# Performance work log

Measured on AMD Instinct MI355X. Metric: run time of the kernel, lower is better.

Reference implementation:

```python
import jax, jax.numpy as jnp
import numpy as np


def setup_inputs() -> dict:
    key = jax.random.key(0)
    k1, k2 = jax.random.split(key)
    B, N, M, D = 8, 4096, 4096, 128
    points1 = jax.random.normal(k1, (B, N, D), dtype=jnp.float32)
    points2 = jax.random.normal(k2, (B, M, D), dtype=jnp.float32)
    return {"points1": points1, "points2": points2}


def reference(points1, points2):
    # sum((x[:, :, None] - y[:, None, :])**2, -1), expressed as a GEMM).
    sq1 = jnp.sum(points1 * points1, axis=-1)              # [B, N]
    sq2 = jnp.sum(points2 * points2, axis=-1)              # [B, M]
    cross = jnp.einsum("bnd,bmd->bnm", points1, points2)   # [B, N, M]
    dist_matrix = sq1[:, :, None] + sq2[:, None, :] - 2.0 * cross
    min_dist1 = jnp.min(dist_matrix, axis=2)               # [B, N]
    min_dist2 = jnp.min(dist_matrix, axis=1)               # [B, M]
    return jnp.mean(min_dist1) + jnp.mean(min_dist2)
```

## Files before the change

### kernel.cpp

```cpp
#include <hip/hip_runtime.h>
#include <hip/hip_bf16.h>


#define BATCH 8
#define NPTS 4096
#define DIM 128
#define FBIAS 16384.0f

using bf16x8 = __attribute__((ext_vector_type(8))) short;
using f32x16 = __attribute__((ext_vector_type(16))) float;

__global__ void prep_kernel(const float* __restrict__ p1,
                            const float* __restrict__ p2,
                            __hip_bfloat16* __restrict__ b1,
                            __hip_bfloat16* __restrict__ b2,
                            float* __restrict__ s1,
                            float* __restrict__ s2) {
    const int arr = blockIdx.y;
    const float* src = arr ? p2 : p1;
    __hip_bfloat16* dst = arr ? b2 : b1;
    float* sq = arr ? s2 : s1;
    const float scale = arr ? 1.0f : -2.0f;

    const int wid = threadIdx.x >> 6;
    const int l   = threadIdx.x & 63;
    const int p   = blockIdx.x * 4 + wid;
    const float2 v = *reinterpret_cast<const float2*>(src + (size_t)p * DIM + l * 2);
    float s = v.x * v.x + v.y * v.y;
    __hip_bfloat162 h = __float22bfloat162_rn(make_float2(v.x * scale, v.y * scale));
    *reinterpret_cast<__hip_bfloat162*>(dst + (size_t)p * DIM + l * 2) = h;
    #pragma unroll
    for (int off = 1; off < 64; off <<= 1) s += __shfl_xor(s, off);
    if (l == 0) sq[p] = s;
}

__device__ __forceinline__ void stage16(const __hip_bfloat16* g, void* lds) {
    __builtin_amdgcn_global_load_lds(
        (const __attribute__((address_space(1))) void*)g,
        (__attribute__((address_space(3))) void*)lds, 16, 0, 0);
}

__global__ void __launch_bounds__(256, 4)
chamfer_tile_kernel(const __hip_bfloat16* __restrict__ bf1,
                    const __hip_bfloat16* __restrict__ bf2,
                    const float* __restrict__ sq1,
                    const float* __restrict__ sq2,
                    unsigned int* __restrict__ min1u,
                    unsigned int* __restrict__ min2u) {
    const int lin = blockIdx.x;
    const int b   = lin & 7;
    const int rest = lin >> 3;
    const int nt  = rest & 31;
    const int mh  = rest >> 5;
    const int tid = threadIdx.x;
    const int wid = tid >> 6;
    const int l   = tid & 63;
    const int l31 = l & 31;
    const int lh  = l >> 5;
    const int base = mh * 1024;

    __shared__ __align__(16) unsigned char btile[2][64 * 256];
    __shared__ unsigned int colminu[1024];

    const __hip_bfloat16* bf1b = bf1 + (size_t)b * NPTS * DIM;
    const __hip_bfloat16* bf2b = bf2 + (size_t)b * NPTS * DIM;
    const float* sq1b = sq1 + b * NPTS;
    const float* sq2b = sq2 + b * NPTS;

    const int n0 = nt * 128 + wid * 32;

    bf16x8 afrag[8];
    #pragma unroll
    for (int ks = 0; ks < 8; ++ks)
        afrag[ks] = *reinterpret_cast<const bf16x8*>(
            bf1b + (n0 + l31) * DIM + ks * 16 + lh * 8);

    float sq1v[16];
    #pragma unroll
    for (int reg = 0; reg < 16; ++reg)
        sq1v[reg] = sq1b[n0 + (reg & 3) + 8 * (reg >> 2) + 4 * lh];

    float rmin[16];
    #pragma unroll
    for (int reg = 0; reg < 16; ++reg) rmin[reg] = 3.4e38f;

    const int bofs = l31 * 256 + ((lh * 16) ^ ((l & 1) << 4));
    const int vks  = (l & 14) << 4;

    auto STAGE = [&](int buf, int m0) {
        #pragma unroll
        for (int j = 0; j < 4; ++j) {
            const int c   = j * 256 + wid * 64 + l;
            const int row = c >> 4;
            const int q   = c & 15;
            const __hip_bfloat16* src =
                bf2b + (size_t)(m0 + row) * DIM + (q ^ (row & 15)) * 8;
            stage16(src, &btile[buf][c * 16]);
        }
    };

    auto TAIL = [&](float cp0, float cp1, int mtIdx) {
        float v0 = fminf(cp0, __shfl_xor(cp0, 32));
        float v1 = fminf(cp1, __shfl_xor(cp1, 32));
        if (l < 32) {
            atomicMin(&colminu[mtIdx * 64 + l], __float_as_uint(v0 + FBIAS));
            atomicMin(&colminu[mtIdx * 64 + 32 + l], __float_as_uint(v1 + FBIAS));
        }
    };

    #pragma unroll
    for (int i = 0; i < 4; ++i) colminu[i * 256 + tid] = 0xFFFFFFFFu;
    STAGE(0, base);

    float cp0 = 3.4e38f, cp1 = 3.4e38f;
    int cur = 0;

    for (int mt = 0; mt < 16; ++mt) {
        const int m0 = base + mt * 64;

        asm volatile("s_barrier" ::: "memory");
        if (mt < 15) STAGE(cur ^ 1, m0 + 64);
        if (mt > 0)  TAIL(cp0, cp1, mt - 1);
        if (mt < 15) asm volatile("s_waitcnt vmcnt(4)\n\ts_barrier" ::: "memory");
        else         asm volatile("s_waitcnt vmcnt(0)\n\ts_barrier" ::: "memory");

        f32x16 acc0 = {}, acc1 = {};
        const unsigned char* bt = &btile[cur][0];
        #pragma unroll
        for (int ks = 0; ks < 8; ++ks) {
            const int ko = ((ks * 32) ^ vks);
            bf16x8 b0 = *reinterpret_cast<const bf16x8*>(&bt[bofs + ko]);
            bf16x8 b1 = *reinterpret_cast<const bf16x8*>(&bt[bofs + ko + 8192]);
            acc0 = __builtin_amdgcn_mfma_f32_32x32x16_bf16(afrag[ks], b0, acc0, 0, 0, 0);
            acc1 = __builtin_amdgcn_mfma_f32_32x32x16_bf16(afrag[ks], b1, acc1, 0, 0, 0);
        }

        const float s2v0 = sq2b[m0 + l31];
        const float s2v1 = sq2b[m0 + 32 + l31];
        #pragma unroll
        for (int reg = 0; reg < 16; ++reg)
            rmin[reg] = fminf(rmin[reg],
                              fminf(acc0[reg] + s2v0, acc1[reg] + s2v1));

        float c0 = 3.4e38f, c1 = 3.4e38f;
        #pragma unroll
        for (int reg = 0; reg < 16; reg += 2) {
            c0 = fminf(c0, fminf(acc0[reg] + sq1v[reg],
                                 acc0[reg + 1] + sq1v[reg + 1]));
            c1 = fminf(c1, fminf(acc1[reg] + sq1v[reg],
                                 acc1[reg + 1] + sq1v[reg + 1]));
        }
        cp0 = c0; cp1 = c1;
        cur ^= 1;
    }

    TAIL(cp0, cp1, 15);
    __syncthreads();

    #pragma unroll
    for (int i = 0; i < 4; ++i) {
        const int c = i * 256 + tid;
        atomicMin(&min2u[(size_t)b * NPTS + base + c], colminu[c]);
    }

    #pragma unroll
    for (int reg = 0; reg < 16; ++reg) {
        float v = rmin[reg];
        v = fminf(v, __shfl_xor(v, 1));
        v = fminf(v, __shfl_xor(v, 2));
        v = fminf(v, __shfl_xor(v, 4));
        v = fminf(v, __shfl_xor(v, 8));
        v = fminf(v, __shfl_xor(v, 16));
        rmin[reg] = v;
    }
    if (l31 == 0) {
        #pragma unroll
        for (int reg = 0; reg < 16; ++reg) {
            const int row = n0 + (reg & 3) + 8 * (reg >> 2) + 4 * lh;
            atomicMin(&min1u[(size_t)b * NPTS + row],
                      __float_as_uint(rmin[reg] + FBIAS));
        }
    }
}

__global__ void finalize_kernel(const unsigned int* __restrict__ min1u,
                                const unsigned int* __restrict__ min2u,
                                const float* __restrict__ sq1,
                                const float* __restrict__ sq2,
                                float* __restrict__ out) {
    const int tid = threadIdx.x;
    const int gid = blockIdx.x * 256 + tid;
    float sum;

    if (gid < BATCH * NPTS) {
        sum = (__uint_as_float(min1u[gid]) - FBIAS + sq1[gid])
              * (1.0f / (BATCH * NPTS));
    } else {
        const int idx = gid - BATCH * NPTS;
        sum = (__uint_as_float(min2u[idx]) - FBIAS + sq2[idx])
              * (1.0f / (BATCH * NPTS));
    }

    #pragma unroll
    for (int off = 1; off < 64; off <<= 1) sum += __shfl_xor(sum, off);
    __shared__ float wsum[4];
    if ((tid & 63) == 0) wsum[tid >> 6] = sum;
    __syncthreads();
    if (tid == 0) atomicAdd(out, wsum[0] + wsum[1] + wsum[2] + wsum[3]);
}

extern "C" void kernel_launch(void* const* d_in, const int* in_sizes, int n_in,
                              void* d_out, int out_size, void* d_ws, size_t ws_size,
                              hipStream_t stream) {
    const float* p1 = (const float*)d_in[0];
    const float* p2 = (const float*)d_in[1];
    float* out = (float*)d_out;

    const size_t npts_tot = (size_t)BATCH * NPTS;
    __hip_bfloat16* bf1 = (__hip_bfloat16*)d_ws;
    __hip_bfloat16* bf2 = bf1 + npts_tot * DIM;
    float* sq1 = (float*)(bf2 + npts_tot * DIM);
    float* sq2 = sq1 + npts_tot;
    unsigned int* min1u = (unsigned int*)(sq2 + npts_tot);
    unsigned int* min2u = min1u + npts_tot;

    hipMemsetAsync(d_out, 0, sizeof(float), stream);
    hipMemsetAsync(min1u, 0xFF, npts_tot * 2 * sizeof(unsigned int), stream);

    prep_kernel<<<dim3(npts_tot / 4, 2), 256, 0, stream>>>(p1, p2, bf1, bf2, sq1, sq2);

    chamfer_tile_kernel<<<1024, 256, 0, stream>>>(bf1, bf2, sq1, sq2, min1u, min2u);

    finalize_kernel<<<256, 256, 0, stream>>>(min1u, min2u, sq1, sq2, out);
}
```

Measured before the change: 138.8 us.

## Fold squared norms into GEMM via augmented K dimension, drop memsets

Pads each point row from 128 to 144 bf16 values. The extra slots hold the squared norm as a bf16 hi/lo pair plus ones, so the MFMA computes the full distance directly. This removes the per-element sq1/sq2 adds and loads in the epilogue, folds the memset initialisation into the prep kernel, and simplifies finalize. The cost is 12.5% more MFMA work and traffic, an unswizzled LDS layout with a 288-byte row stride that may raise bank conflicts, and some loss of precision from the bf16 split norms.

```diff
diff --git a/kernel.cpp b/kernel.cpp
--- a/kernel.cpp
+++ b/kernel.cpp
@@ -5,6 +5,8 @@
 #define BATCH 8
 #define NPTS 4096
 #define DIM 128
+#define DIME 144
+#define ROWB 288
 #define FBIAS 16384.0f
 
 using bf16x8 = __attribute__((ext_vector_type(8))) short;
@@ -14,27 +16,49 @@
                             const float* __restrict__ p2,
                             __hip_bfloat16* __restrict__ b1,
                             __hip_bfloat16* __restrict__ b2,
-                            float* __restrict__ s1,
-                            float* __restrict__ s2) {
+                            unsigned int* __restrict__ minAll,
+                            float* __restrict__ out) {
     const int arr = blockIdx.y;
     const float* src = arr ? p2 : p1;
     __hip_bfloat16* dst = arr ? b2 : b1;
-    float* sq = arr ? s2 : s1;
     const float scale = arr ? 1.0f : -2.0f;
 
     const int wid = threadIdx.x >> 6;
     const int l   = threadIdx.x & 63;
     const int p   = blockIdx.x * 4 + wid;
+
     const float2 v = *reinterpret_cast<const float2*>(src + (size_t)p * DIM + l * 2);
     float s = v.x * v.x + v.y * v.y;
     __hip_bfloat162 h = __float22bfloat162_rn(make_float2(v.x * scale, v.y * scale));
-    *reinterpret_cast<__hip_bfloat162*>(dst + (size_t)p * DIM + l * 2) = h;
+    *reinterpret_cast<__hip_bfloat162*>(dst + (size_t)p * DIME + l * 2) = h;
     #pragma unroll
     for (int off = 1; off < 64; off <<= 1) s += __shfl_xor(s, off);
-    if (l == 0) sq[p] = s;
-}
-
-__device__ __forceinline__ void stage16(const __hip_bfloat16* g, void* lds) {
+
+    if (l < 8) {
+        const __hip_bfloat16 shi = __float2bfloat16(s);
+        const __hip_bfloat16 slo = __float2bfloat16(s - __bfloat162float(shi));
+        const __hip_bfloat16 one = __float2bfloat16(1.0f);
+        const __hip_bfloat16 zero = __float2bfloat16(0.0f);
+        __hip_bfloat16 a = zero, bb = zero;
+        if (arr == 0) {
+            if (l == 0) { a = shi; bb = slo; }
+            else if (l == 1) { a = one; bb = one; }
+        } else {
+            if (l == 0) { a = one; bb = one; }
+            else if (l == 1) { a = shi; bb = slo; }
+        }
+        __hip_bfloat162 pair; pair.x = a; pair.y = bb;
+        *reinterpret_cast<__hip_bfloat162*>(dst + (size_t)p * DIME + DIM + l * 2) = pair;
+    }
+
+    if (arr == 0) {
+        if (threadIdx.x < 8)
+            minAll[blockIdx.x * 8 + threadIdx.x] = 0xFFFFFFFFu;
+        if (blockIdx.x == 0 && threadIdx.x == 0) out[0] = 0.0f;
+    }
+}
+
+__device__ __forceinline__ void stage16(const void* g, void* lds) {
     __builtin_amdgcn_global_load_lds(
         (const __attribute__((address_space(1))) void*)g,
         (__attribute__((address_space(3))) void*)lds, 16, 0, 0);
@@ -43,8 +67,6 @@
 __global__ void __launch_bounds__(256, 4)
 chamfer_tile_kernel(const __hip_bfloat16* __restrict__ bf1,
                     const __hip_bfloat16* __restrict__ bf2,
-                    const float* __restrict__ sq1,
-                    const float* __restrict__ sq2,
                     unsigned int* __restrict__ min1u,
                     unsigned int* __restrict__ min2u) {
     const int lin = blockIdx.x;
@@ -59,43 +81,33 @@
     const int lh  = l >> 5;
     const int base = mh * 1024;
 
-    __shared__ __align__(16) unsigned char btile[2][64 * 256];
+    __shared__ __align__(16) unsigned char btile[2][64 * ROWB];
     __shared__ unsigned int colminu[1024];
 
-    const __hip_bfloat16* bf1b = bf1 + (size_t)b * NPTS * DIM;
-    const __hip_bfloat16* bf2b = bf2 + (size_t)b * NPTS * DIM;
-    const float* sq1b = sq1 + b * NPTS;
-    const float* sq2b = sq2 + b * NPTS;
+    const unsigned char* bf1b = (const unsigned char*)(bf1) + (size_t)b * NPTS * ROWB;
+    const unsigned char* bf2b = (const unsigned char*)(bf2) + (size_t)b * NPTS * ROWB;
 
     const int n0 = nt * 128 + wid * 32;
 
-    bf16x8 afrag[8];
-    #pragma unroll
-    for (int ks = 0; ks < 8; ++ks)
+    bf16x8 afrag[9];
+    #pragma unroll
+    for (int ks = 0; ks < 9; ++ks)
         afrag[ks] = *reinterpret_cast<const bf16x8*>(
-            bf1b + (n0 + l31) * DIM + ks * 16 + lh * 8);
-
-    float sq1v[16];
-    #pragma unroll
-    for (int reg = 0; reg < 16; ++reg)
-        sq1v[reg] = sq1b[n0 + (reg & 3) + 8 * (reg >> 2) + 4 * lh];
+            bf1b + (size_t)(n0 + l31) * ROWB + ks * 32 + lh * 16);
 
     float rmin[16];
     #pragma unroll
     for (int reg = 0; reg < 16; ++reg) rmin[reg] = 3.4e38f;
 
-    const int bofs = l31 * 256 + ((lh * 16) ^ ((l & 1) << 4));
-    const int vks  = (l & 14) << 4;
+    const int bofs = l31 * ROWB + lh * 16;
 
     auto STAGE = [&](int buf, int m0) {
-        #pragma unroll
-        for (int j = 0; j < 4; ++j) {
-            const int c   = j * 256 + wid * 64 + l;
-            const int row = c >> 4;
-            const int q   = c & 15;
-            const __hip_bfloat16* src =
-                bf2b + (size_t)(m0 + row) * DIM + (q ^ (row & 15)) * 8;
-            stage16(src, &btile[buf][c * 16]);
+        const unsigned char* tb = bf2b + (size_t)m0 * ROWB;
+        #pragma unroll
+        for (int j = 0; j < 5; ++j) {
+            int c = j * 256 + tid;
+            c = (c >= 1152) ? (c - 1152) : c;
+            stage16(tb + c * 16, &btile[buf][c * 16]);
         }
     };
 
@@ -121,36 +133,34 @@
         asm volatile("s_barrier" ::: "memory");
         if (mt < 15) STAGE(cur ^ 1, m0 + 64);
         if (mt > 0)  TAIL(cp0, cp1, mt - 1);
-        if (mt < 15) asm volatile("s_waitcnt vmcnt(4)\n\ts_barrier" ::: "memory");
+        if (mt < 15) asm volatile("s_waitcnt vmcnt(5)\n\ts_barrier" ::: "memory");
         else         asm volatile("s_waitcnt vmcnt(0)\n\ts_barrier" ::: "memory");
 
         f32x16 acc0 = {}, acc1 = {};
         const unsigned char* bt = &btile[cur][0];
         #pragma unroll
-        for (int ks = 0; ks < 8; ++ks) {
-            const int ko = ((ks * 32) ^ vks);
-            bf16x8 b0 = *reinterpret_cast<const bf16x8*>(&bt[bofs + ko]);
-            bf16x8 b1 = *reinterpret_cast<const bf16x8*>(&bt[bofs + ko + 8192]);
+        for (int ks = 0; ks < 9; ++ks) {
+            bf16x8 b0 = *reinterpret_cast<const bf16x8*>(&bt[bofs + ks * 32]);
+            bf16x8 b1 = *reinterpret_cast<const bf16x8*>(&bt[bofs + ks * 32 + 32 * ROWB]);
             acc0 = __builtin_amdgcn_mfma_f32_32x32x16_bf16(afrag[ks], b0, acc0, 0, 0, 0);
             acc1 = __builtin_amdgcn_mfma_f32_32x32x16_bf16(afrag[ks], b1, acc1, 0, 0, 0);
         }
 
-        const float s2v0 = sq2b[m0 + l31];
-        const float s2v1 = sq2b[m0 + 32 + l31];
         #pragma unroll
         for (int reg = 0; reg < 16; ++reg)
-            rmin[reg] = fminf(rmin[reg],
-                              fminf(acc0[reg] + s2v0, acc1[reg] + s2v1));
-
-        float c0 = 3.4e38f, c1 = 3.4e38f;
-        #pragma unroll
-        for (int reg = 0; reg < 16; reg += 2) {
-            c0 = fminf(c0, fminf(acc0[reg] + sq1v[reg],
-                                 acc0[reg + 1] + sq1v[reg + 1]));
-            c1 = fminf(c1, fminf(acc1[reg] + sq1v[reg],
-                                 acc1[reg + 1] + sq1v[reg + 1]));
-        }
-        cp0 = c0; cp1 = c1;
+            rmin[reg] = fminf(rmin[reg], fminf(acc0[reg], acc1[reg]));
+
+        float c0a = fminf(fminf(acc0[0], acc0[1]), fminf(acc0[2], acc0[3]));
+        float c0b = fminf(fminf(acc0[4], acc0[5]), fminf(acc0[6], acc0[7]));
+        float c0c = fminf(fminf(acc0[8], acc0[9]), fminf(acc0[10], acc0[11]));
+        float c0d = fminf(fminf(acc0[12], acc0[13]), fminf(acc0[14], acc0[15]));
+        cp0 = fminf(fminf(c0a, c0b), fminf(c0c, c0d));
+        float c1a = fminf(fminf(acc1[0], acc1[1]), fminf(acc1[2], acc1[3]));
+        float c1b = fminf(fminf(acc1[4], acc1[5]), fminf(acc1[6], acc1[7]));
+        float c1c = fminf(fminf(acc1[8], acc1[9]), fminf(acc1[10], acc1[11]));
+        float c1d = fminf(fminf(acc1[12], acc1[13]), fminf(acc1[14], acc1[15]));
+        cp1 = fminf(fminf(c1a, c1b), fminf(c1c, c1d));
+
         cur ^= 1;
     }
 
@@ -183,23 +193,12 @@
     }
 }
 
-__global__ void finalize_kernel(const unsigned int* __restrict__ min1u,
-                                const unsigned int* __restrict__ min2u,
-                                const float* __restrict__ sq1,
-                                const float* __restrict__ sq2,
+__global__ void finalize_kernel(const unsigned int* __restrict__ minAll,
                                 float* __restrict__ out) {
     const int tid = threadIdx.x;
     const int gid = blockIdx.x * 256 + tid;
-    float sum;
-
-    if (gid < BATCH * NPTS) {
-        sum = (__uint_as_float(min1u[gid]) - FBIAS + sq1[gid])
-              * (1.0f / (BATCH * NPTS));
-    } else {
-        const int idx = gid - BATCH * NPTS;
-        sum = (__uint_as_float(min2u[idx]) - FBIAS + sq2[idx])
-              * (1.0f / (BATCH * NPTS));
-    }
+    float sum = (__uint_as_float(minAll[gid]) - FBIAS)
+                * (1.0f / (BATCH * NPTS));
 
     #pragma unroll
     for (int off = 1; off < 64; off <<= 1) sum += __shfl_xor(sum, off);
@@ -217,19 +216,13 @@
     float* out = (float*)d_out;
 
     const size_t npts_tot = (size_t)BATCH * NPTS;
-    __hip_bfloat16* bf1 = (__hip_bfloat16*)d_ws;
-    __hip_bfloat16* bf2 = bf1 + npts_tot * DIM;
-    float* sq1 = (float*)(bf2 + npts_tot * DIM);
-    float* sq2 = sq1 + npts_tot;
-    unsigned int* min1u = (unsigned int*)(sq2 + npts_tot);
+    __hip_bfloat16* bf1e = (__hip_bfloat16*)d_ws;
+    __hip_bfloat16* bf2e = bf1e + npts_tot * DIME;
+    unsigned int* min1u = (unsigned int*)(bf2e + npts_tot * DIME);
     unsigned int* min2u = min1u + npts_tot;
 
-    hipMemsetAsync(d_out, 0, sizeof(float), stream);
-    hipMemsetAsync(min1u, 0xFF, npts_tot * 2 * sizeof(unsigned int), stream);
-
-    prep_kernel<<<dim3(npts_tot / 4, 2), 256, 0, stream>>>(p1, p2, bf1, bf2, sq1, sq2);
-
-    chamfer_tile_kernel<<<1024, 256, 0, stream>>>(bf1, bf2, sq1, sq2, min1u, min2u);
-
-    finalize_kernel<<<256, 256, 0, stream>>>(min1u, min2u, sq1, sq2, out);
-}
+    prep_kernel<<<dim3(npts_tot / 4, 2), 256, 0, stream>>>(p1, p2, bf1e, bf2e,
+                                                           min1u, out);
+    chamfer_tile_kernel<<<1024, 256, 0, stream>>>(bf1e, bf2e, min1u, min2u);
+    finalize_kernel<<<256, 256, 0, stream>>>(min1u, out);
+}
```

Measured after the change: 124.6 us. 10.2% less time.
